# Optimization experiments

Measured on AMD Instinct MI355X. Metric: run time of the kernel, lower is better.

The kernel has to match this reference:

```python
import jax, jax.numpy as jnp
import numpy as np

DIM = 192; HEADS = 6; HD = DIM // HEADS; SCALE = HD ** -0.5
WS = (4, 8, 8); SS = (2, 4, 4)
NW = WS[0] * WS[1] * WS[2]  # tokens per window = 256
HIDDEN = 768; RANK1 = 384; RANK2 = 96

def _rel_index():
    Wd, Wh, Ww = WS
    coords = np.stack(np.meshgrid(np.arange(Wd), np.arange(Wh), np.arange(Ww), indexing='ij')).reshape(3, -1)
    rel = (coords[:, :, None] - coords[:, None, :]).transpose(1, 2, 0)
    rel = rel + np.array([Wd - 1, Wh - 1, Ww - 1])
    rel[:, :, 0] *= (2 * Wh - 1) * (2 * Ww - 1)
    rel[:, :, 1] *= 2 * Ww - 1
    return rel.sum(-1)  # (NW, NW) int

REL_IDX = jnp.asarray(_rel_index())

def _attn_mask(B, D, H, W):
    # static numpy computation (D,H,W are python ints) -> constant under jit
    img = np.zeros((B, D, H, W), np.float32); cnt = 0
    for d in range(0, D, WS[0]):
        for h in range(0, H, WS[1]):
            for w in range(0, W, WS[2]):
                img[:, d:d + WS[0], h:h + WS[1], w:w + WS[2]] = cnt; cnt += 1
    if any(s > 0 for s in SS):
        img = np.roll(img, (-SS[0], -SS[1], -SS[2]), axis=(1, 2, 3))
    mw = img.reshape(B, D // WS[0], WS[0], H // WS[1], WS[1], W // WS[2], WS[2]).transpose(0, 1, 3, 5, 2, 4, 6).reshape(-1, NW)
    diff = mw[:, :, None] - mw[:, None, :]
    return jnp.asarray(np.where(diff != 0, -100.0, 0.0).astype(np.float32))  # (B*nW, NW, NW)

def _ln(x, g, b):
    mu = x.mean(-1, keepdims=True)
    var = ((x - mu) ** 2).mean(-1, keepdims=True)
    return (x - mu) / jnp.sqrt(var + 1e-5) * g + b

def setup_inputs() -> dict:
    key = jax.random.key(0)
    ks = jax.random.split(key, 16)
    B, D, H, W = 1, 16, 64, 64
    N = D * H * W
    s = 0.02
    return {
        'x': jax.random.normal(ks[0], (B, N, DIM), jnp.float32),
        'norm1_g': jnp.ones((DIM,), jnp.float32), 'norm1_b': jnp.zeros((DIM,), jnp.float32),
        'qkv_w': jax.random.normal(ks[1], (DIM, 3 * DIM), jnp.float32) * s,
        'qkv_b': jnp.zeros((3 * DIM,), jnp.float32),
        'rel_bias': jax.random.normal(ks[2], (1575, HEADS), jnp.float32) * s,
        'proj_w': jax.random.normal(ks[3], (DIM, DIM), jnp.float32) * s,
        'proj_b': jnp.zeros((DIM,), jnp.float32),
        'norm2_g': jnp.ones((DIM,), jnp.float32), 'norm2_b': jnp.zeros((DIM,), jnp.float32),
        'fc1_A': jax.random.normal(ks[4], (DIM, RANK1), jnp.float32) * s,
        'fc1_Bw': jax.random.normal(ks[5], (RANK1, HIDDEN), jnp.float32) * s,
        'fc1_Bb': jnp.zeros((HIDDEN,), jnp.float32),
        'dw_w': jax.random.normal(ks[6], (HIDDEN, 1, 3, 3, 3), jnp.float32) * s,
        'dw_b': jnp.zeros((HIDDEN,), jnp.float32),
        'fc2_A': jax.random.normal(ks[7], (HIDDEN, RANK2), jnp.float32) * s,
        'fc2_Bw': jax.random.normal(ks[8], (RANK2, DIM), jnp.float32) * s,
        'fc2_Bb': jnp.zeros((DIM,), jnp.float32),
        'D': D, 'H': H, 'W': W,
    }

def reference(x, norm1_g, norm1_b, qkv_w, qkv_b, rel_bias, proj_w, proj_b,
              norm2_g, norm2_b, fc1_A, fc1_Bw, fc1_Bb, dw_w, dw_b,
              fc2_A, fc2_Bw, fc2_Bb, D, H, W):
    B, N, C = x.shape
    Wd, Wh, Ww = WS
    shortcut = x
    # --- shifted-window attention (NB: original repo never rolls x; only the mask is shifted) ---
    h = _ln(x, norm1_g, norm1_b).reshape(B, D, H, W, C)
    xw = h.reshape(B, D // Wd, Wd, H // Wh, Wh, W // Ww, Ww, C)
    xw = xw.transpose(0, 1, 3, 5, 2, 4, 6, 7).reshape(-1, NW, C)  # (B*nW, NW, C)
    qkv = (xw @ qkv_w + qkv_b).reshape(-1, NW, 3, HEADS, HD).transpose(2, 0, 3, 1, 4)
    q, k, v = qkv[0] * SCALE, qkv[1], qkv[2]           # (B*nW, heads, NW, hd)
    attn = jnp.einsum('bhnd,bhmd->bhnm', q, k)
    bias = rel_bias[REL_IDX].transpose(2, 0, 1)[None]  # (1, heads, NW, NW)
    mask = _attn_mask(B, D, H, W)                      # (B*nW, NW, NW)
    attn = jax.nn.softmax(attn + bias + mask[:, None], axis=-1)
    out = jnp.einsum('bhnm,bhmd->bhnd', attn, v).transpose(0, 2, 1, 3).reshape(-1, NW, C)
    out = out @ proj_w + proj_b
    out = out.reshape(B, D // Wd, H // Wh, W // Ww, Wd, Wh, Ww, C)
    out = out.transpose(0, 1, 4, 2, 5, 3, 6, 7).reshape(B, N, C)
    x = shortcut + out
    # --- MixFFN3D: low-rank fc1 -> depthwise conv3d -> GELU -> low-rank fc2 ---
    h = _ln(x, norm2_g, norm2_b)
    h = (h @ fc1_A) @ fc1_Bw + fc1_Bb                 # (B, N, HIDDEN)
    h = h.transpose(0, 2, 1).reshape(B, HIDDEN, D, H, W)
    h = jax.lax.conv_general_dilated(h, dw_w, (1, 1, 1), [(1, 1), (1, 1), (1, 1)],
                                     feature_group_count=HIDDEN,
                                     dimension_numbers=('NCDHW', 'OIDHW', 'NCDHW'))
    h = h + dw_b[None, :, None, None, None]
    h = jax.nn.gelu(h, approximate=False)
    h = h.reshape(B, HIDDEN, N).transpose(0, 2, 1)
    h = (h @ fc2_A) @ fc2_Bw + fc2_Bb                 # (B, N, DIM)
    return x + h
```

## Files before the change

kernel.cpp:

```cpp
#include <hip/hip_runtime.h>
#include <hip/hip_bf16.h>
#include <hip/hip_fp16.h>

typedef __hip_bfloat16 bf16;
typedef __attribute__((ext_vector_type(8))) short short8;
typedef __attribute__((ext_vector_type(8))) _Float16 half8;
typedef __attribute__((ext_vector_type(4))) float f32x4;

#define N_TOK 65536
#define C_DIM 192
#define SCALE 0.17677669529663687f

__device__ __forceinline__ float b2f(bf16 v) { return __bfloat162float(v); }
__device__ __forceinline__ bf16 f2b(float v) { return __float2bfloat16(v); }
__device__ __forceinline__ float ldA(const void* p, size_t i, int f32) {
  return f32 ? ((const float*)p)[i] : b2f(((const bf16*)p)[i]);
}
__device__ __forceinline__ float s2f(short s) { union { short s; bf16 b; } u; u.s = s; return b2f(u.b); }

__device__ __forceinline__ float gelu_f(float s) {
  float t = s * s;
  float b = s * (-1.59576912f - 0.0713548162f * t);
  float e = __expf(b);
  return s / (1.f + e);
}

__global__ void detect_kernel(const unsigned short* __restrict__ xh, int* __restrict__ flag) {
  if (threadIdx.x == 0) {
    int crazy = 0;
    for (int i = 0; i < 256; ++i) {
      int e = (xh[i] >> 7) & 0xFF;
      if (e >= 0xF0 || (e >= 1 && e <= 0x60)) ++crazy;
    }
    *flag = (crazy >= 16) ? 1 : 0;
  }
}

__global__ __launch_bounds__(256) void prep_xpose_kernel(
    const void* __restrict__ qkv_w, bf16* __restrict__ QKVT,
    const void* __restrict__ proj_w, bf16* __restrict__ PROJT,
    const void* __restrict__ dw_w, _Float16* __restrict__ DWT,
    const void* __restrict__ fc1_A, bf16* __restrict__ FC1AB,
    const void* __restrict__ fc1_Bw, bf16* __restrict__ FC1BWT,
    const void* __restrict__ fc2_A, bf16* __restrict__ FC2AB,
    const void* __restrict__ fc2_Bw, bf16* __restrict__ FC2BWT,
    const int* __restrict__ flag) {
  int f32 = *flag;
  int b = blockIdx.x;
  if (b < 432) {
    int idx = b * 256 + threadIdx.x;
    int n = idx / 192, k = idx - n * 192;
    QKVT[idx] = f2b(ldA(qkv_w, (size_t)k * 576 + n, f32));
  } else if (b < 576) {
    int idx = (b - 432) * 256 + threadIdx.x;
    int n = idx / 192, k = idx - n * 192;
    PROJT[idx] = f2b(ldA(proj_w, (size_t)k * 192 + n, f32));
  } else if (b < 657) {
    int idx = (b - 576) * 256 + threadIdx.x;
    int tap = idx / 768, c = idx - tap * 768;
    DWT[idx] = (_Float16)ldA(dw_w, (size_t)c * 27 + tap, f32);
  } else if (b < 945) {
    int idx = (b - 657) * 256 + threadIdx.x;
    FC1AB[idx] = f2b(ldA(fc1_A, idx, f32));
  } else if (b < 2097) {
    int idx = (b - 945) * 256 + threadIdx.x;
    int n = idx / 384, r = idx - n * 384;
    FC1BWT[idx] = f2b(ldA(fc1_Bw, (size_t)r * 768 + n, f32));
  } else if (b < 2385) {
    int idx = (b - 2097) * 256 + threadIdx.x;
    FC2AB[idx] = f2b(ldA(fc2_A, idx, f32));
  } else {
    int idx = (b - 2385) * 256 + threadIdx.x;
    int n = idx / 96, r = idx - n * 96;
    FC2BWT[idx] = f2b(ldA(fc2_Bw, (size_t)r * 192 + n, f32));
  }
}

__global__ __launch_bounds__(256) void ln_kernel(const void* __restrict__ x,
    const void* __restrict__ g, const void* __restrict__ b, bf16* __restrict__ out,
    int windowize, int xIsBf16Fixed, const int* __restrict__ flag) {
  int wf32 = *flag;
  int f32 = xIsBf16Fixed ? 0 : wf32;
  int token = blockIdx.x * 4 + (threadIdx.x >> 6);
  int lane = threadIdx.x & 63;
  size_t base = (size_t)token * C_DIM;
  float v0 = ldA(x, base + lane, f32);
  float v1 = ldA(x, base + lane + 64, f32);
  float v2 = ldA(x, base + lane + 128, f32);
  float s = v0 + v1 + v2;
  float s2 = v0 * v0 + v1 * v1 + v2 * v2;
  #pragma unroll
  for (int o = 32; o > 0; o >>= 1) { s += __shfl_xor(s, o, 64); s2 += __shfl_xor(s2, o, 64); }
  float mu = s * (1.f / 192.f);
  float var = s2 * (1.f / 192.f) - mu * mu;
  float rstd = rsqrtf(var + 1e-5f);
  int row = token;
  if (windowize) {
    int d = token >> 12, h = (token >> 6) & 63, w = token & 63;
    int win = ((d >> 2) << 6) + ((h >> 3) << 3) + (w >> 3);
    int t = ((d & 3) << 6) + ((h & 7) << 3) + (w & 7);
    row = win * 256 + t;
  }
  bf16* po = out + (size_t)row * C_DIM;
  po[lane]       = f2b((v0 - mu) * rstd * ldA(g, lane, wf32)       + ldA(b, lane, wf32));
  po[lane + 64]  = f2b((v1 - mu) * rstd * ldA(g, lane + 64, wf32)  + ldA(b, lane + 64, wf32));
  po[lane + 128] = f2b((v2 - mu) * rstd * ldA(g, lane + 128, wf32) + ldA(b, lane + 128, wf32));
}

template<int F16>
__global__ __launch_bounds__(256) void mfma_gemm(const bf16* __restrict__ A,
    const bf16* __restrict__ BT, const void* __restrict__ bias,
    const void* __restrict__ res, void* __restrict__ out,
    int Nc, int K, int ldk, int mode, int Mrows, const int* __restrict__ flag) {
  int f32 = *flag;
  __shared__ short As[128 * 96];
  __shared__ short Bs[64 * 96];
  int tid = threadIdx.x;
  int wave = tid >> 6, lane = tid & 63;
  int wm = wave >> 1, wn = wave & 1;
  int lr = lane & 15, quad = lane >> 4;
  int rowBase, colBase;
  if (gridDim.y >= 8) {
    int ncb = gridDim.x;
    int flat = blockIdx.x + ncb * blockIdx.y;
    int group = flat / (8 * ncb);
    int r = flat - group * 8 * ncb;
    rowBase = (group * 8 + (r & 7)) * 128;
    colBase = (r >> 3) * 64;
  } else {
    rowBase = blockIdx.y * 128;
    colBase = blockIdx.x * 64;
  }
  f32x4 acc[4][2];
  #pragma unroll
  for (int i = 0; i < 4; ++i)
    #pragma unroll
    for (int j = 0; j < 2; ++j) acc[i][j] = f32x4{0.f, 0.f, 0.f, 0.f};

  const bf16* arow = A + (size_t)rowBase * K;
  const bf16* brow = BT + (size_t)colBase * ldk;

  for (int k0 = 0; k0 < K; k0 += 96) {
    #pragma unroll
    for (int it = 0; it < 6; ++it) {
      int u = tid + it * 256;
      int row = u / 12, kc = (u - row * 12) * 8;
      __builtin_amdgcn_global_load_lds(
          (const __attribute__((address_space(1))) void*)(arow + (size_t)row * K + k0 + kc),
          (__attribute__((address_space(3))) void*)&As[u * 8], 16, 0, 0);
    }
    #pragma unroll
    for (int it = 0; it < 3; ++it) {
      int u = tid + it * 256;
      int n = u / 12, kc = (u - n * 12) * 8;
      __builtin_amdgcn_global_load_lds(
          (const __attribute__((address_space(1))) void*)(brow + (size_t)n * ldk + k0 + kc),
          (__attribute__((address_space(3))) void*)&Bs[u * 8], 16, 0, 0);
    }
    __syncthreads();
    #pragma unroll
    for (int kk = 0; kk < 3; ++kk) {
      short8 af[4], bf[2];
      #pragma unroll
      for (int i = 0; i < 4; ++i)
        af[i] = *(const short8*)&As[(wm * 64 + i * 16 + lr) * 96 + kk * 32 + quad * 8];
      #pragma unroll
      for (int j = 0; j < 2; ++j)
        bf[j] = *(const short8*)&Bs[(wn * 32 + j * 16 + lr) * 96 + kk * 32 + quad * 8];
      #pragma unroll
      for (int i = 0; i < 4; ++i)
        #pragma unroll
        for (int j = 0; j < 2; ++j) {
          if constexpr (F16) {
            union { short8 s; half8 h; } ua, ub;
            ua.s = af[i]; ub.s = bf[j];
            acc[i][j] = __builtin_amdgcn_mfma_f32_16x16x32_f16(ua.h, ub.h, acc[i][j], 0, 0, 0);
          } else {
            acc[i][j] = __builtin_amdgcn_mfma_f32_16x16x32_bf16(af[i], bf[j], acc[i][j], 0, 0, 0);
          }
        }
    }
    __syncthreads();
  }

  #pragma unroll
  for (int i = 0; i < 4; ++i) {
    #pragma unroll
    for (int j = 0; j < 2; ++j) {
      #pragma unroll
      for (int r4 = 0; r4 < 4; ++r4) {
        int row = rowBase + wm * 64 + i * 16 + quad * 4 + r4;
        int c = colBase + wn * 32 + j * 16 + lr;
        if (c >= Nc || row >= Mrows) continue;
        float v = acc[i][j][r4];
        if (bias) v += ldA(bias, c, f32);
        if (mode == 0) {
          ((bf16*)out)[(size_t)row * Nc + c] = f2b(v);
        } else if (mode == 1) {
          float o = b2f(((const bf16*)res)[(size_t)row * Nc + c]) + v;
          if (f32) ((float*)out)[(size_t)row * Nc + c] = o;
          else     ((bf16*)out)[(size_t)row * Nc + c] = f2b(o);
        } else if (mode == 4) {
          ((bf16*)out)[(size_t)c * Mrows + row] = f2b(v);
        } else if (mode == 5) {
          ((_Float16*)out)[(size_t)row * Nc + c] = (_Float16)v;
        } else if (mode == 6) {
          ((_Float16*)out)[(size_t)c * Mrows + row] = (_Float16)v;
        } else {
          int win = row >> 8, t = row & 255;
          int d = ((win >> 6) << 2) + (t >> 6);
          int h = (((win >> 3) & 7) << 3) + ((t >> 3) & 7);
          int w = ((win & 7) << 3) + (t & 7);
          int n = (d << 12) + (h << 6) + w;
          ((bf16*)out)[(size_t)n * C_DIM + c] = f2b(ldA(res, (size_t)n * C_DIM + c, f32) + v);
        }
      }
    }
  }
}

__global__ __launch_bounds__(256) void attn_mfma_kernel(const bf16* __restrict__ qkvr,
    const void* __restrict__ rel_bias, bf16* __restrict__ out,
    const int* __restrict__ flag) {
  int f32 = *flag;
  __shared__ bf16 sK[256 * 40];
  __shared__ bf16 sVT[32 * 264];
  __shared__ bf16 sP[4][64 * 40];
  __shared__ float sb[1575];
  __shared__ int  sgb[256];
  int head = blockIdx.x, win = blockIdx.y;
  const bf16* base = qkvr + (size_t)win * 256 * 576;
  int qoff = head * 32, koff = 192 + head * 32, voff = 384 + head * 32;
  int tid = threadIdx.x;
  int wave = tid >> 6, lane = tid & 63;
  int lr = lane & 15, quad = lane >> 4;

  #pragma unroll
  for (int it = 0; it < 4; ++it) {
    int idx = tid + it * 256;
    int tok = idx >> 2, kc = (idx & 3) * 8;
    uint4 v = *(const uint4*)(base + (size_t)tok * 576 + koff + kc);
    *(uint4*)&sK[tok * 40 + kc] = v;
  }
  for (int idx = tid; idx < 8192; idx += 256) {
    int tok = idx >> 5, hd = idx & 31;
    sVT[hd * 264 + tok] = base[(size_t)tok * 576 + voff + hd];
  }
  for (int idx = tid; idx < 1575; idx += 256) sb[idx] = ldA(rel_bias, (size_t)idx * 6 + head, f32);
  {
    int t = tid & 255;
    int d = ((win >> 6) << 2) + (t >> 6);
    int h = (((win >> 3) & 7) << 3) + ((t >> 3) & 7);
    int w = ((win & 7) << 3) + (t & 7);
    int d2 = (d + 2) & 15, h2 = (h + 4) & 63, w2 = (w + 4) & 63;
    int g = ((d2 >> 2) << 6) + ((h2 >> 3) << 3) + (w2 >> 3);
    int td = t >> 6, th = (t >> 3) & 7, tw = t & 7;
    int bse = (td * 15 + th) * 15 + tw;
    sgb[t] = (g << 12) | bse;
  }
  __syncthreads();

  int wm = wave * 64;
  short8 aq[4];
  #pragma unroll
  for (int i = 0; i < 4; ++i)
    aq[i] = *(const short8*)(base + (size_t)(wm + i * 16 + lr) * 576 + qoff + quad * 8);
  int rinfo[16];
  #pragma unroll
  for (int i = 0; i < 4; ++i)
    #pragma unroll
    for (int r = 0; r < 4; ++r)
      rinfo[i * 4 + r] = sgb[wm + i * 16 + quad * 4 + r];

  f32x4 acc_o[4][2], acc_l[4];
  #pragma unroll
  for (int i = 0; i < 4; ++i) {
    acc_l[i] = f32x4{0.f, 0.f, 0.f, 0.f};
    #pragma unroll
    for (int j = 0; j < 2; ++j) acc_o[i][j] = f32x4{0.f, 0.f, 0.f, 0.f};
  }
  short8 bones;
  #pragma unroll
  for (int j = 0; j < 8; ++j) bones[j] = (lr == 0) ? (short)0x3F80 : (short)0;

  for (int c = 0; c < 8; ++c) {
    short8 bk[2];
    #pragma unroll
    for (int jt = 0; jt < 2; ++jt)
      bk[jt] = *(const short8*)&sK[(c * 32 + jt * 16 + lr) * 40 + quad * 8];
    f32x4 s[4][2];
    #pragma unroll
    for (int i = 0; i < 4; ++i)
      #pragma unroll
      for (int jt = 0; jt < 2; ++jt) {
        s[i][jt] = f32x4{0.f, 0.f, 0.f, 0.f};
        s[i][jt] = __builtin_amdgcn_mfma_f32_16x16x32_bf16(aq[i], bk[jt], s[i][jt], 0, 0, 0);
      }
    int cinfo[2];
    #pragma unroll
    for (int jt = 0; jt < 2; ++jt) cinfo[jt] = sgb[c * 32 + jt * 16 + lr];
    #pragma unroll
    for (int i = 0; i < 4; ++i)
      #pragma unroll
      for (int jt = 0; jt < 2; ++jt)
        #pragma unroll
        for (int r = 0; r < 4; ++r) {
          int ri = rinfo[i * 4 + r], ci = cinfo[jt];
          float sc = s[i][jt][r] * SCALE + sb[(ri & 0xFFF) - (ci & 0xFFF) + 787];
          float p = ((ri >> 12) == (ci >> 12)) ? __expf(sc) : 0.f;
          sP[wave][(i * 16 + quad * 4 + r) * 40 + jt * 16 + lr] = f2b(p);
        }
    short8 ap[4];
    #pragma unroll
    for (int i = 0; i < 4; ++i)
      ap[i] = *(const short8*)&sP[wave][(i * 16 + lr) * 40 + quad * 8];
    short8 bv[2];
    #pragma unroll
    for (int jh = 0; jh < 2; ++jh)
      bv[jh] = *(const short8*)&sVT[(jh * 16 + lr) * 264 + c * 32 + quad * 8];
    #pragma unroll
    for (int i = 0; i < 4; ++i) {
      #pragma unroll
      for (int jh = 0; jh < 2; ++jh)
        acc_o[i][jh] = __builtin_amdgcn_mfma_f32_16x16x32_bf16(ap[i], bv[jh], acc_o[i][jh], 0, 0, 0);
      acc_l[i] = __builtin_amdgcn_mfma_f32_16x16x32_bf16(ap[i], bones, acc_l[i], 0, 0, 0);
    }
  }
  #pragma unroll
  for (int i = 0; i < 4; ++i) {
    #pragma unroll
    for (int r = 0; r < 4; ++r) {
      float l = __shfl(acc_l[i][r], lane & 48, 64);
      float inv = 1.f / l;
      int t = wm + i * 16 + quad * 4 + r;
      bf16* po = out + (size_t)(win * 256 + t) * C_DIM + head * 32;
      po[lr]      = f2b(acc_o[i][0][r] * inv);
      po[16 + lr] = f2b(acc_o[i][1][r] * inv);
    }
  }
}

__global__ __launch_bounds__(256, 8) void dwconv_f16_kernel(const _Float16* __restrict__ in,
    const _Float16* __restrict__ wT, const void* __restrict__ wb, _Float16* __restrict__ out,
    const int* __restrict__ flag) {
  int f32 = *flag;
  int vb = (blockIdx.x & 7) * (gridDim.x >> 3) + (blockIdx.x >> 3);
  int idx = vb * 256 + threadIdx.x;
  int q = idx / 96, g = idx - q * 96;
  int c0 = g * 8;
  int d = q & 15, h = (q >> 4) & 63, w0 = (q >> 10) << 2;
  const _Float16* inb = in + c0;
  half8 acc[4];
  #pragma unroll
  for (int t = 0; t < 4; ++t)
    #pragma unroll
    for (int e = 0; e < 8; ++e) acc[t][e] = (_Float16)0.f;
  #pragma unroll
  for (int kd = 0; kd < 3; ++kd) {
    int dd = d + kd - 1;
    if ((unsigned)dd >= 16u) continue;
    #pragma unroll
    for (int kh = 0; kh < 3; ++kh) {
      int hh = h + kh - 1;
      if ((unsigned)hh >= 64u) continue;
      int rowbase = (dd << 12) + (hh << 6);
      half8 xf[6];
      #pragma unroll
      for (int j = 0; j < 6; ++j) {
        int ww = w0 + j - 1;
        if ((unsigned)ww < 64u) {
          xf[j] = *(const half8*)(inb + (size_t)(rowbase + ww) * 768);
        } else {
          #pragma unroll
          for (int e = 0; e < 8; ++e) xf[j][e] = (_Float16)0.f;
        }
      }
      #pragma unroll
      for (int kw = 0; kw < 3; ++kw) {
        int tap = kd * 9 + kh * 3 + kw;
        half8 wv = *(const half8*)(wT + tap * 768 + c0);
        #pragma unroll
        for (int t = 0; t < 4; ++t)
          acc[t] += xf[t + kw] * wv;
      }
    }
  }
  float biasf[8];
  #pragma unroll
  for (int e = 0; e < 8; ++e) biasf[e] = ldA(wb, c0 + e, f32);
  #pragma unroll
  for (int t = 0; t < 4; ++t) {
    half8 po;
    #pragma unroll
    for (int e = 0; e < 8; ++e) {
      float s = (float)acc[t][e] + biasf[e];
      po[e] = (_Float16)gelu_f(s);
    }
    *(half8*)(out + (size_t)((d << 12) + (h << 6) + w0 + t) * 768 + c0) = po;
  }
}

extern "C" void kernel_launch(void* const* d_in, const int* in_sizes, int n_in,
                              void* d_out, int out_size, void* d_ws, size_t ws_size,
                              hipStream_t stream) {
  const void* x      = d_in[0];
  const void* n1g    = d_in[1];
  const void* n1b    = d_in[2];
  const void* qkv_w  = d_in[3];
  const void* qkv_b  = d_in[4];
  const void* relb   = d_in[5];
  const void* proj_w = d_in[6];
  const void* proj_b = d_in[7];
  const void* n2g    = d_in[8];
  const void* n2b    = d_in[9];
  const void* fc1_A  = d_in[10];
  const void* fc1_Bw = d_in[11];
  const void* fc1_Bb = d_in[12];
  const void* dw_w   = d_in[13];
  const void* dw_b   = d_in[14];
  const void* fc2_A  = d_in[15];
  const void* fc2_Bw = d_in[16];
  const void* fc2_Bb = d_in[17];

  char* ws = (char*)d_ws;
  bf16* SCR  = (bf16*)d_out;
  bf16* X1   = (bf16*)(ws);
  bf16* QKVR = (bf16*)(ws + (size_t)24 * 1048576);
  _Float16* F2 = (_Float16*)(ws + (size_t)24 * 1048576);
  _Float16* F1 = (_Float16*)(ws + (size_t)120 * 1048576);
  bf16* QKVT   = (bf16*)(ws + (size_t)228 * 1048576);
  bf16* PROJT  = (bf16*)(ws + (size_t)229 * 1048576);
  _Float16* DWT = (_Float16*)(ws + (size_t)230 * 1048576);
  bf16* W1T    = (bf16*)(ws + (size_t)231 * 1048576);
  _Float16* W2T = (_Float16*)(ws + (size_t)232 * 1048576);
  bf16* FC1AB  = (bf16*)(ws + (size_t)233 * 1048576);
  bf16* FC1BWT = (bf16*)(ws + (size_t)234 * 1048576);
  bf16* FC2AB  = (bf16*)(ws + (size_t)236 * 1048576);
  bf16* FC2BWT = (bf16*)(ws + (size_t)237 * 1048576);
  int* FLAG    = (int*)(ws + (size_t)255 * 1048576);

  detect_kernel<<<1, 64, 0, stream>>>((const unsigned short*)x, FLAG);
  prep_xpose_kernel<<<2457, 256, 0, stream>>>(qkv_w, QKVT, proj_w, PROJT, dw_w, DWT,
                                              fc1_A, FC1AB, fc1_Bw, FC1BWT,
                                              fc2_A, FC2AB, fc2_Bw, FC2BWT, FLAG);
  mfma_gemm<0><<<dim3(12, 2), 256, 0, stream>>>(FC1AB, FC1BWT, nullptr, nullptr, W1T,
                                                768, 384, 384, 4, 192, FLAG);
  mfma_gemm<0><<<dim3(3, 6), 256, 0, stream>>>(FC2AB, FC2BWT, nullptr, nullptr, W2T,
                                               192, 96, 96, 6, 768, FLAG);
  ln_kernel<<<N_TOK / 4, 256, 0, stream>>>(x, n1g, n1b, SCR, 1, 0, FLAG);
  mfma_gemm<0><<<dim3(9, 512), 256, 0, stream>>>(SCR, QKVT, qkv_b, nullptr, QKVR,
                                                 576, 192, 192, 0, N_TOK, FLAG);
  attn_mfma_kernel<<<dim3(6, 256), 256, 0, stream>>>(QKVR, relb, SCR, FLAG);
  mfma_gemm<0><<<dim3(3, 512), 256, 0, stream>>>(SCR, PROJT, proj_b, x, X1,
                                                 192, 192, 192, 3, N_TOK, FLAG);
  ln_kernel<<<N_TOK / 4, 256, 0, stream>>>(X1, n2g, n2b, SCR, 0, 1, FLAG);
  mfma_gemm<0><<<dim3(12, 512), 256, 0, stream>>>(SCR, W1T, fc1_Bb, nullptr, F1,
                                                  768, 192, 192, 5, N_TOK, FLAG);
  dwconv_f16_kernel<<<6144, 256, 0, stream>>>(F1, DWT, dw_b, F2, FLAG);
  mfma_gemm<1><<<dim3(3, 512), 256, 0, stream>>>((const bf16*)F2, (const bf16*)W2T,
                                                 fc2_Bb, X1, d_out,
                                                 192, 768, 768, 1, N_TOK, FLAG);
}
```

Before: 668.8 us.

## Fuse depthwise conv + GELU with fc2 GEMM and residual in one kernel

Replaces the separate depthwise-conv kernel and the fc2 GEMM with one kernel. Each block computes conv+GELU for 16 tokens into LDS, then multiplies by the fused fc2 weight with MFMA f16 and adds bias and residual. This removes the write and re-read of the 768-wide intermediate F2 (about 100MB of traffic) and one launch. In exchange the conv work is split into smaller per-block tiles with more halo reloads, the GEMM uses M=16 per block, and W2 is reloaded from L2 for every block with a sync at each k-step.

After: 705.9 us. 1.06x slower.

```diff
diff --git a/kernel.cpp b/kernel.cpp
--- a/kernel.cpp
+++ b/kernel.cpp
@@ -340,63 +340,127 @@
   }
 }
 
-__global__ __launch_bounds__(256, 8) void dwconv_f16_kernel(const _Float16* __restrict__ in,
-    const _Float16* __restrict__ wT, const void* __restrict__ wb, _Float16* __restrict__ out,
+__global__ __launch_bounds__(256) void dwfc2_kernel(const _Float16* __restrict__ F1,
+    const _Float16* __restrict__ wT, const void* __restrict__ dwb,
+    const _Float16* __restrict__ W2, const void* __restrict__ fc2b,
+    const bf16* __restrict__ X1, void* __restrict__ out,
     const int* __restrict__ flag) {
   int f32 = *flag;
+  __shared__ _Float16 As[16 * 776];
+  __shared__ _Float16 Bs[192 * 64];
+  int tid = threadIdx.x;
   int vb = (blockIdx.x & 7) * (gridDim.x >> 3) + (blockIdx.x >> 3);
-  int idx = vb * 256 + threadIdx.x;
-  int q = idx / 96, g = idx - q * 96;
-  int c0 = g * 8;
-  int d = q & 15, h = (q >> 4) & 63, w0 = (q >> 10) << 2;
-  const _Float16* inb = in + c0;
-  half8 acc[4];
-  #pragma unroll
-  for (int t = 0; t < 4; ++t)
-    #pragma unroll
-    for (int e = 0; e < 8; ++e) acc[t][e] = (_Float16)0.f;
-  #pragma unroll
-  for (int kd = 0; kd < 3; ++kd) {
-    int dd = d + kd - 1;
-    if ((unsigned)dd >= 16u) continue;
-    #pragma unroll
-    for (int kh = 0; kh < 3; ++kh) {
-      int hh = h + kh - 1;
-      if ((unsigned)hh >= 64u) continue;
-      int rowbase = (dd << 12) + (hh << 6);
-      half8 xf[6];
-      #pragma unroll
-      for (int j = 0; j < 6; ++j) {
-        int ww = w0 + j - 1;
-        if ((unsigned)ww < 64u) {
-          xf[j] = *(const half8*)(inb + (size_t)(rowbase + ww) * 768);
-        } else {
-          #pragma unroll
-          for (int e = 0; e < 8; ++e) xf[j][e] = (_Float16)0.f;
+  int nbase = vb * 16;
+  int d = nbase >> 12, h = (nbase >> 6) & 63, wb = nbase & 63;
+
+  #pragma unroll
+  for (int it = 0; it < 6; ++it) {
+    int u = tid + it * 256;
+    int n = u >> 3, c16 = u & 7;
+    int cs = c16 ^ (n & 7);
+    __builtin_amdgcn_global_load_lds(
+        (const __attribute__((address_space(1))) void*)(W2 + (size_t)n * 768 + cs * 8),
+        (__attribute__((address_space(3))) void*)&Bs[u * 8], 16, 0, 0);
+  }
+
+  #pragma unroll
+  for (int ti = 0; ti < 3; ++ti) {
+    int tt = tid + ti * 256;
+    int q2 = tt / 96, g = tt - q2 * 96;
+    int c0 = g * 8;
+    int w0 = wb + q2 * 2;
+    half8 acc[2];
+    #pragma unroll
+    for (int t = 0; t < 2; ++t)
+      #pragma unroll
+      for (int e = 0; e < 8; ++e) acc[t][e] = (_Float16)0.f;
+    #pragma unroll
+    for (int kd = 0; kd < 3; ++kd) {
+      int dd = d + kd - 1;
+      if ((unsigned)dd >= 16u) continue;
+      #pragma unroll
+      for (int kh = 0; kh < 3; ++kh) {
+        int hh = h + kh - 1;
+        if ((unsigned)hh >= 64u) continue;
+        int rowbase = (dd << 12) + (hh << 6);
+        half8 xf[4];
+        #pragma unroll
+        for (int j = 0; j < 4; ++j) {
+          int ww = w0 + j - 1;
+          if ((unsigned)ww < 64u) {
+            xf[j] = *(const half8*)(F1 + (size_t)(rowbase + ww) * 768 + c0);
+          } else {
+            #pragma unroll
+            for (int e = 0; e < 8; ++e) xf[j][e] = (_Float16)0.f;
+          }
+        }
+        #pragma unroll
+        for (int kw = 0; kw < 3; ++kw) {
+          half8 wv = *(const half8*)(wT + (kd * 9 + kh * 3 + kw) * 768 + c0);
+          acc[0] += xf[kw] * wv;
+          acc[1] += xf[kw + 1] * wv;
         }
       }
-      #pragma unroll
-      for (int kw = 0; kw < 3; ++kw) {
-        int tap = kd * 9 + kh * 3 + kw;
-        half8 wv = *(const half8*)(wT + tap * 768 + c0);
-        #pragma unroll
-        for (int t = 0; t < 4; ++t)
-          acc[t] += xf[t + kw] * wv;
+    }
+    #pragma unroll
+    for (int t = 0; t < 2; ++t) {
+      half8 po;
+      #pragma unroll
+      for (int e = 0; e < 8; ++e) {
+        float s = (float)acc[t][e] + ldA(dwb, c0 + e, f32);
+        po[e] = (_Float16)gelu_f(s);
       }
-    }
-  }
-  float biasf[8];
-  #pragma unroll
-  for (int e = 0; e < 8; ++e) biasf[e] = ldA(wb, c0 + e, f32);
-  #pragma unroll
-  for (int t = 0; t < 4; ++t) {
-    half8 po;
-    #pragma unroll
-    for (int e = 0; e < 8; ++e) {
-      float s = (float)acc[t][e] + biasf[e];
-      po[e] = (_Float16)gelu_f(s);
-    }
-    *(half8*)(out + (size_t)((d << 12) + (h << 6) + w0 + t) * 768 + c0) = po;
+      *(half8*)&As[(q2 * 2 + t) * 776 + c0] = po;
+    }
+  }
+  __syncthreads();
+
+  int wave = tid >> 6, lane = tid & 63;
+  int lr = lane & 15, quad = lane >> 4;
+  f32x4 acc2[3];
+  #pragma unroll
+  for (int j = 0; j < 3; ++j) acc2[j] = f32x4{0.f, 0.f, 0.f, 0.f};
+
+  for (int k0 = 0; k0 < 768; k0 += 64) {
+    #pragma unroll
+    for (int kk = 0; kk < 2; ++kk) {
+      half8 af = *(const half8*)&As[lr * 776 + k0 + kk * 32 + quad * 8];
+      #pragma unroll
+      for (int j = 0; j < 3; ++j) {
+        int n = wave * 48 + j * 16 + lr;
+        int cs = (kk * 4 + quad) ^ (n & 7);
+        half8 bf = *(const half8*)&Bs[n * 64 + cs * 8];
+        acc2[j] = __builtin_amdgcn_mfma_f32_16x16x32_f16(af, bf, acc2[j], 0, 0, 0);
+      }
+    }
+    __syncthreads();
+    if (k0 + 64 < 768) {
+      int k1 = k0 + 64;
+      #pragma unroll
+      for (int it = 0; it < 6; ++it) {
+        int u = tid + it * 256;
+        int n = u >> 3, c16 = u & 7;
+        int cs = c16 ^ (n & 7);
+        __builtin_amdgcn_global_load_lds(
+            (const __attribute__((address_space(1))) void*)(W2 + (size_t)n * 768 + k1 + cs * 8),
+            (__attribute__((address_space(3))) void*)&Bs[u * 8], 16, 0, 0);
+      }
+      __syncthreads();
+    }
+  }
+
+  #pragma unroll
+  for (int j = 0; j < 3; ++j) {
+    int c = wave * 48 + j * 16 + lr;
+    float bv = ldA(fc2b, c, f32);
+    #pragma unroll
+    for (int r4 = 0; r4 < 4; ++r4) {
+      int row = quad * 4 + r4;
+      size_t oi = (size_t)(nbase + row) * C_DIM + c;
+      float o = b2f(X1[oi]) + acc2[j][r4] + bv;
+      if (f32) ((float*)out)[oi] = o;
+      else     ((bf16*)out)[oi] = f2b(o);
+    }
   }
 }
 
@@ -426,7 +490,6 @@
   bf16* SCR  = (bf16*)d_out;
   bf16* X1   = (bf16*)(ws);
   bf16* QKVR = (bf16*)(ws + (size_t)24 * 1048576);
-  _Float16* F2 = (_Float16*)(ws + (size_t)24 * 1048576);
   _Float16* F1 = (_Float16*)(ws + (size_t)120 * 1048576);
   bf16* QKVT   = (bf16*)(ws + (size_t)228 * 1048576);
   bf16* PROJT  = (bf16*)(ws + (size_t)229 * 1048576);
@@ -456,8 +519,5 @@
   ln_kernel<<<N_TOK / 4, 256, 0, stream>>>(X1, n2g, n2b, SCR, 0, 1, FLAG);
   mfma_gemm<0><<<dim3(12, 512), 256, 0, stream>>>(SCR, W1T, fc1_Bb, nullptr, F1,
                                                   768, 192, 192, 5, N_TOK, FLAG);
-  dwconv_f16_kernel<<<6144, 256, 0, stream>>>(F1, DWT, dw_b, F2, FLAG);
-  mfma_gemm<1><<<dim3(3, 512), 256, 0, stream>>>((const bf16*)F2, (const bf16*)W2T,
-                                                 fc2_Bb, X1, d_out,
-                                                 192, 768, 768, 1, N_TOK, FLAG);
-}
+  dwfc2_kernel<<<4096, 256, 0, stream>>>(F1, DWT, dw_b, W2T, fc2_Bb, X1, d_out, FLAG);
+}
```
